# Optimization experiments

Measured on AMD Instinct MI355X. Metric: run time of the kernel, lower is better.

Reference implementation:

```python
import jax, jax.numpy as jnp
import numpy as np

N, E, B = 2048, 65536, 8
H, G, F, S, MH, L = 128, 50, 64, 16, 32, 2
K = 512                       # = master_rate * N
CUTOFF = 10.0
TAU = 1.0
LAMBDA_ATTN = 0.002
OFFSET = jnp.linspace(0.0, CUTOFF, G)
COEFF = -0.5 / (CUTOFF / (G - 1)) ** 2


def ssp(x):
    # shifted softplus used by SchNet
    return jax.nn.softplus(x) - jnp.log(2.0)


def gauss(d):
    # GaussianSmearing: exp(coeff * (d - offset)^2)
    return jnp.exp(COEFF * (d[..., None] - OFFSET) ** 2)


def ccut(d):
    # cosine cutoff of CFConv
    return 0.5 * (jnp.cos(d * jnp.pi / CUTOFF) + 1.0)


def dist(a, b):
    # eps keeps sqrt grad finite at coincident points / self edges
    return jnp.sqrt(jnp.sum((a - b) ** 2, axis=-1) + 1e-12)


def filt(ea, mw1, mb1, mw2, mb2):
    # CFConv filter network on edge_attr
    return ssp(ea @ mw1 + mb1) @ mw2 + mb2


def hmp_layer(h, pos, src, dst, p):
    (mw1, mb1, mw2, mb2, cf1, cf2w, cf2b, lw, lb,
     aw1, ab1, aw2, ab2, msw1, msb1, msw2, msb2, wq, wk) = p
    # ---- local SchNet interaction over the full edge list (decay = 1) ----
    d = dist(pos[src], pos[dst])                                    # [E]
    W = filt(gauss(d), mw1, mb1, mw2, mb2) * ccut(d)[:, None]       # [E,F]
    x = h @ cf1                                                     # [N,F]
    agg = jnp.zeros((N, F), h.dtype).at[dst].add(x[src] * W)
    h_local = h + (ssp(agg @ cf2w + cf2b) @ lw + lb)
    # ---- master selection (top-K on scalar channels, soft sigmoid gate) ----
    hs = h_local[:, :S]
    scores = jax.nn.relu(hs @ msw1 + msb1) @ msw2 + msb2            # [N]
    topv, topi = jax.lax.top_k(scores, K)
    m = jax.nn.sigmoid((scores - topv[K - 1] + 1e-6) / TAU)         # m>0.5 exactly for masters
    midx = jnp.sort(topi)
    is_m = jnp.zeros((N,), bool).at[midx].set(True)
    inv = jnp.zeros((N,), jnp.int32).at[midx].set(jnp.arange(K, dtype=jnp.int32))
    valid = is_m[src] & is_m[dst]                                   # induced-subgraph edges
    srcm = jnp.where(valid, inv[src], 0)
    dstm = jnp.where(valid, inv[dst], 0)
    vf = valid.astype(h.dtype)
    adj = jnp.zeros((K, K), h.dtype).at[srcm, dstm].add(vf) > 0     # to_dense_adj
    h_m, pos_m = h_local[midx], pos[midx]
    # ---- virtual edge generation (dot-product attention, thresholded) ----
    hms = h_m[:, :S]
    attn = jax.nn.softmax((hms @ wq) @ (hms @ wk).T / jnp.sqrt(jnp.asarray(S, h.dtype)), axis=-1)
    Av = ((attn > LAMBDA_ATTN) & ~adj & ~jnp.eye(K, dtype=bool)).astype(h.dtype)  # [K,K]
    # ---- master interaction: induced edges (sparse) + virtual edges (dense) ----
    dm = dist(pos_m[srcm], pos_m[dstm])
    Wm = filt(gauss(dm), mw1, mb1, mw2, mb2) * (ccut(dm) * vf)[:, None]
    xm = h_m @ cf1                                                  # [K,F]
    agg_s = jnp.zeros((K, F), h.dtype).at[dstm].add(xm[srcm] * Wm)
    dmat = dist(pos_m[:, None, :], pos_m[None, :, :])               # [K,K]
    gmat = gauss(dmat)                                              # [K,K,G]
    Wi, Wj, Wd = aw1[:H], aw1[H:2 * H], aw1[2 * H:]                 # split concat-MLP first layer
    pre = jax.nn.relu((h_m @ Wi)[:, None, :] + (h_m @ Wj)[None, :, :] + gmat @ Wd + ab1)
    score = pre @ aw2 + ab2                                         # [K,K] attn_mlp score
    # scatter_softmax grouped by source row over existing virtual edges
    decay = jax.nn.softmax(jnp.where(Av > 0, score, -1e9), axis=1) * Av
    Wv = filt(gmat * decay[..., None], mw1, mb1, mw2, mb2) * (ccut(dmat) * Av)[..., None]
    agg_d = jnp.einsum('if,ijf->jf', xm, Wv)                        # aggregate at target col
    h_hier = h_m + (ssp((agg_s + agg_d) @ cf2w + cf2b) @ lw + lb)
    h_exp = jnp.zeros_like(h_local).at[midx].set(h_hier)
    mc = m[:, None]
    return (1.0 - mc) * h_local + mc * h_exp


def reference(atoms, pos, src, dst, batch, emb,
              ib_mlp_w1, ib_mlp_b1, ib_mlp_w2, ib_mlp_b2,
              cf_lin1_w, cf_lin2_w, cf_lin2_b, ib_lin_w, ib_lin_b,
              attn_w1, attn_b1, attn_w2, attn_b2,
              ms_w1, ms_b1, ms_w2, ms_b2, vg_wq, vg_wk,
              pred_w1, pred_b1, pred_w2, pred_b2):
    ps = (ib_mlp_w1, ib_mlp_b1, ib_mlp_w2, ib_mlp_b2,
          cf_lin1_w, cf_lin2_w, cf_lin2_b, ib_lin_w, ib_lin_b,
          attn_w1, attn_b1, attn_w2, attn_b2,
          ms_w1, ms_b1, ms_w2, ms_b2, vg_wq, vg_wk)
    h = emb[atoms]
    for l in range(L):
        h = hmp_layer(h, pos, src, dst, tuple(q[l] for q in ps))
    pooled = jax.ops.segment_sum(h, batch, num_segments=B)          # global_add_pool
    return jax.nn.silu(pooled @ pred_w1 + pred_b1) @ pred_w2 + pred_b2


def setup_inputs():
    key = jax.random.key(0)
    ks = jax.random.split(key, 20)
    def rn(i, shape, s):
        return jax.random.normal(ks[i], shape, jnp.float32) * s
    return {
        'atoms': jax.random.randint(ks[0], (N,), 0, 100),
        'pos': jax.random.normal(ks[1], (N, 3), jnp.float32) * 3.0,
        'src': jax.random.randint(ks[2], (E,), 0, N),
        'dst': jax.random.randint(ks[3], (E,), 0, N),
        'batch': (jnp.arange(N) * B) // N,
        'emb': rn(4, (100, H), 0.5),
        'ib_mlp_w1': rn(5, (L, G, F), 0.1),
        'ib_mlp_b1': jnp.zeros((L, F), jnp.float32),
        'ib_mlp_w2': rn(6, (L, F, F), 0.1),
        'ib_mlp_b2': jnp.zeros((L, F), jnp.float32),
        'cf_lin1_w': rn(7, (L, H, F), 0.05),
        'cf_lin2_w': rn(8, (L, F, H), 0.05),
        'cf_lin2_b': jnp.zeros((L, H), jnp.float32),
        'ib_lin_w': rn(9, (L, H, H), 0.05),
        'ib_lin_b': jnp.zeros((L, H), jnp.float32),
        'attn_w1': rn(10, (L, 2 * H + G, H), 0.05),
        'attn_b1': jnp.zeros((L, H), jnp.float32),
        'attn_w2': rn(11, (L, H), 0.05),
        'attn_b2': jnp.zeros((L,), jnp.float32),
        'ms_w1': rn(12, (L, S, MH), 0.2),
        'ms_b1': jnp.zeros((L, MH), jnp.float32),
        'ms_w2': rn(13, (L, MH), 0.2),
        'ms_b2': jnp.zeros((L,), jnp.float32),
        'vg_wq': rn(14, (L, S, S), 0.2),
        'vg_wk': rn(15, (L, S, S), 0.2),
        'pred_w1': rn(16, (H, H // 2), 0.05),
        'pred_b1': jnp.zeros((H // 2,), jnp.float32),
        'pred_w2': rn(17, (H // 2, 1), 0.05),
        'pred_b2': jnp.zeros((1,), jnp.float32),
    }
```

## Files before the change

### kernel.cpp

```cpp
#include <hip/hip_runtime.h>
#include <hip/hip_bf16.h>
#include <math.h>

#define N_ATOMS 2048
#define E_EDGES 65536
#define B_BATCH 8
#define H_DIM 128
#define G_DIM 50
#define F_DIM 64
#define S_DIM 16
#define MH_DIM 32
#define K_TOP 512
#define L_LAYERS 2
#define EPW2 8
#define PCHUNK 8
#define NB 4096
#define DD 0.015625f
#define INV_DD 64.0f

static constexpr float STEP   = 10.0f / 49.0f;
static constexpr float COEFF  = -12.005f;
static constexpr float PI10   = 0.31415926535897931f;
static constexpr float LN2    = 0.69314718055994531f;
static constexpr float LAMBDA = 0.002f;

#define DEV static __device__ __forceinline__

DEV float ssp_f(float x) { return fmaxf(x, 0.f) + log1pf(expf(-fabsf(x))) - LN2; }
DEV float ccut_f(float d) { return 0.5f * (cosf(d * PI10) + 1.f); }
DEV float sigm_f(float x) { return 1.f / (1.f + expf(-x)); }
DEV float ssp_fast(float x) { return fmaxf(x, 0.f) + __logf(1.f + __expf(-fabsf(x))) - LN2; }
DEV float ccut_fast(float d) { return 0.5f * (__cosf(d * PI10) + 1.f); }

__global__ __launch_bounds__(256) void k_detect(const unsigned short* raw, int n, int* flag) {
    __shared__ int any;
    if (threadIdx.x == 0) any = 0;
    __syncthreads();
    for (int i = threadIdx.x; i < n; i += 256) {
        unsigned int bits = ((unsigned int)raw[i]) << 16;
        float f = __uint_as_float(bits);
        if (!(fabsf(f) <= 1e10f)) any = 1;
    }
    __syncthreads();
    if (threadIdx.x == 0) flag[0] = any;
}

struct ConvArgs {
    const void* p[25];
    int off[26];
};

__global__ __launch_bounds__(256) void k_convert_all(ConvArgs a, float* dst, const int* flag) {
    int i = blockIdx.x * 256 + threadIdx.x;
    int total = a.off[25];
    if (i >= total) return;
    int seg = 0;
    while (i >= a.off[seg + 1]) seg++;
    int k = i - a.off[seg];
    if (flag[0]) {
        dst[i] = ((const float*)a.p[seg])[k];
    } else {
        unsigned int bits = ((unsigned int)((const unsigned short*)a.p[seg])[k]) << 16;
        dst[i] = __uint_as_float(bits);
    }
}

__global__ __launch_bounds__(256) void k_ehist(const int* dst, int* hist) {
    int e = blockIdx.x * 256 + threadIdx.x;
    atomicAdd(&hist[dst[e]], 1);
}

__global__ __launch_bounds__(1024) void k_escan(const int* hist, int* ebase, int* ecur) {
    __shared__ int bufA[N_ATOMS], bufB[N_ATOMS];
    int t = threadIdx.x;
    for (int i = t; i < N_ATOMS; i += 1024) bufA[i] = hist[i];
    __syncthreads();
    int* in = bufA;
    int* out = bufB;
    for (int d = 1; d < N_ATOMS; d <<= 1) {
        for (int i = t; i < N_ATOMS; i += 1024) out[i] = in[i] + (i >= d ? in[i - d] : 0);
        __syncthreads();
        int* tmp = in; in = out; out = tmp;
    }
    for (int i = t; i < N_ATOMS; i += 1024) {
        int ex = in[i] - hist[i];
        ebase[i] = ex;
        ecur[i] = ex;
    }
}

__global__ __launch_bounds__(256) void k_escatter(const int* dst, int* ecur, int* esorted) {
    int e = blockIdx.x * 256 + threadIdx.x;
    int pos = atomicAdd(&ecur[dst[e]], 1);
    esorted[pos] = e;
}

__global__ __launch_bounds__(256) void k_edat(const int* esorted, const int* src, const int* dst,
                                              const float* pos, int4* edat) {
    int p = blockIdx.x * 256 + threadIdx.x;
    int e = esorted[p];
    int s = src[e], d = dst[e];
    float dx = pos[s * 3 + 0] - pos[d * 3 + 0];
    float dy = pos[s * 3 + 1] - pos[d * 3 + 1];
    float dz = pos[s * 3 + 2] - pos[d * 3 + 2];
    float dist = sqrtf(dx * dx + dy * dy + dz * dz + 1e-12f);
    edat[p] = make_int4(s, d, __float_as_int(dist), 0);
}

__global__ __launch_bounds__(128) void k_ftab(const float* mw1, const float* mb1,
                                              const float* mw2, const float* mb2,
                                              const float* aw1,
                                              float* z1tab, float* wtab, float* ztabS) {
    __shared__ float gs[G_DIM];
    __shared__ float tb[F_DIM];
    int b = blockIdx.x, t = threadIdx.x;
    float d = b * DD;
    if (t < G_DIM) { float u = d - t * STEP; gs[t] = expf(COEFF * u * u); }
    __syncthreads();
    const float* wd = aw1 + 2 * H_DIM * H_DIM;
    float zs = 0.f;
    for (int g = 0; g < G_DIM; g++) zs += gs[g] * wd[g * H_DIM + t];
    ztabS[b * H_DIM + t] = zs;
    if (t < F_DIM) {
        float z1 = 0.f;
        for (int g = 0; g < G_DIM; g++) z1 += gs[g] * mw1[g * F_DIM + t];
        z1tab[b * F_DIM + t] = z1;
        tb[t] = ssp_f(z1 + mb1[t]);
    }
    __syncthreads();
    if (t < F_DIM) {
        float w = mb2[t];
        for (int k = 0; k < F_DIM; k++) w += tb[k] * mw2[k * F_DIM + t];
        wtab[b * F_DIM + t] = w * ccut_f(d);
    }
}

__global__ __launch_bounds__(256) void k_embed(const int* atoms, const float* emb, float* h) {
    int i = blockIdx.x * 256 + threadIdx.x;
    int n = i >> 7, c = i & 127;
    h[i] = emb[atoms[n] * H_DIM + c];
}

__global__ __launch_bounds__(256) void k_x(const float* __restrict__ h, const float* __restrict__ cf1,
                                           float* __restrict__ x, float* __restrict__ aggz, int M) {
    int wave = threadIdx.x >> 6, lane = threadIdx.x & 63;
    int n = blockIdx.x * 4 + wave;
    if (n >= M) return;
    float acc = 0.f;
    for (int k = 0; k < H_DIM; k++) acc += h[n * H_DIM + k] * cf1[k * F_DIM + lane];
    x[n * F_DIM + lane] = acc;
    aggz[n * F_DIM + lane] = 0.f;
}

__global__ __launch_bounds__(256) void k_edge_s(const int4* edat, const float* x,
                                                const float* __restrict__ wtab,
                                                float* agg) {
    int t = threadIdx.x, wave = t >> 6, lane = t & 63;
    int p0 = (blockIdx.x * 4 + wave) * EPW2;
    int curDst = -1;
    float acc = 0.f;
    for (int ee = 0; ee < EPW2; ee++) {
        int4 ed = edat[p0 + ee];
        int sI = ed.x, dI = ed.y;
        float d = __int_as_float(ed.z);
        float s = d * INV_DD;
        int b0 = min((int)s, NB - 2);
        float fr = s - b0;
        float w0 = wtab[b0 * F_DIM + lane];
        float w1 = wtab[(b0 + 1) * F_DIM + lane];
        float w = w0 + fr * (w1 - w0);
        float contrib = x[sI * F_DIM + lane] * w;
        if (dI != curDst) {
            if (curDst >= 0) atomicAdd(&agg[curDst * F_DIM + lane], acc);
            acc = 0.f;
            curDst = dI;
        }
        acc += contrib;
    }
    if (curDst >= 0) atomicAdd(&agg[curDst * F_DIM + lane], acc);
}

__global__ __launch_bounds__(256) void k_update(const float* __restrict__ agg, const float* __restrict__ base,
                                                const float* cf2w, const float* cf2b,
                                                const float* lw, const float* lb,
                                                float* out, int M) {
    __shared__ float tbuf[4][H_DIM];
    int wave = threadIdx.x >> 6, lane = threadIdx.x & 63;
    int n = blockIdx.x * 4 + wave;
    float t0 = cf2b[lane], t1 = cf2b[lane + 64];
    if (n < M) {
        for (int f = 0; f < F_DIM; f++) {
            float a = agg[n * F_DIM + f];
            t0 += a * cf2w[f * H_DIM + lane];
            t1 += a * cf2w[f * H_DIM + lane + 64];
        }
    }
    tbuf[wave][lane] = ssp_f(t0);
    tbuf[wave][lane + 64] = ssp_f(t1);
    __syncthreads();
    if (n < M) {
        float o0 = lb[lane], o1 = lb[lane + 64];
        const float4* t4v = (const float4*)tbuf[wave];
        #pragma unroll
        for (int kk = 0; kk < 32; kk++) {
            float4 tq = t4v[kk];
            int k4 = kk * 4;
            o0 += tq.x * lw[(k4 + 0) * H_DIM + lane];
            o1 += tq.x * lw[(k4 + 0) * H_DIM + lane + 64];
            o0 += tq.y * lw[(k4 + 1) * H_DIM + lane];
            o1 += tq.y * lw[(k4 + 1) * H_DIM + lane + 64];
            o0 += tq.z * lw[(k4 + 2) * H_DIM + lane];
            o1 += tq.z * lw[(k4 + 2) * H_DIM + lane + 64];
            o0 += tq.w * lw[(k4 + 3) * H_DIM + lane];
            o1 += tq.w * lw[(k4 + 3) * H_DIM + lane + 64];
        }
        out[n * H_DIM + lane]      = base[n * H_DIM + lane] + o0;
        out[n * H_DIM + lane + 64] = base[n * H_DIM + lane + 64] + o1;
    }
}

__global__ __launch_bounds__(256) void k_scores(const float* h_local,
                                                const float* msw1, const float* msb1,
                                                const float* msw2, const float* msb2,
                                                float* scores) {
    int n = blockIdx.x * 256 + threadIdx.x;
    if (n >= N_ATOMS) return;
    float hs[S_DIM];
    for (int s = 0; s < S_DIM; s++) hs[s] = h_local[n * H_DIM + s];
    float sc = msb2[0];
    for (int j = 0; j < MH_DIM; j++) {
        float v = msb1[j];
        for (int s = 0; s < S_DIM; s++) v += hs[s] * msw1[s * MH_DIM + j];
        sc += fmaxf(v, 0.f) * msw2[j];
    }
    scores[n] = sc;
}

__global__ __launch_bounds__(256) void k_rank(const float* scores, int* rank) {
    __shared__ float s[N_ATOMS];
    __shared__ int pc[16][17];
    int t = threadIdx.x;
    for (int i = t; i < N_ATOMS; i += 256) s[i] = scores[i];
    __syncthreads();
    int ii = t & 15, chunk = t >> 4;
    int i = blockIdx.x * 16 + ii;
    float si = s[i];
    int cnt = 0;
    int j0 = chunk * (N_ATOMS / 16);
    #pragma unroll 4
    for (int j = j0; j < j0 + N_ATOMS / 16; j++) {
        float sj = s[j];
        cnt += (sj > si) || (sj == si && j < i);
    }
    pc[chunk][ii] = cnt;
    __syncthreads();
    if (chunk == 0) {
        int r = 0;
        #pragma unroll
        for (int c = 0; c < 16; c++) r += pc[c][ii];
        rank[i] = r;
    }
}

__global__ __launch_bounds__(1024) void k_select(const float* scores, const int* rank,
                                                 int* is_m, int* invg, int* midx, float* m) {
    __shared__ int flag[N_ATOMS];
    __shared__ int bufA[N_ATOMS], bufB[N_ATOMS];
    __shared__ float kth;
    int t = threadIdx.x;
    for (int i = t; i < N_ATOMS; i += 1024) {
        int f = rank[i] < K_TOP;
        flag[i] = f;
        bufA[i] = f;
        if (rank[i] == K_TOP - 1) kth = scores[i];
    }
    __syncthreads();
    int* in = bufA;
    int* out = bufB;
    for (int d = 1; d < N_ATOMS; d <<= 1) {
        for (int i = t; i < N_ATOMS; i += 1024) out[i] = in[i] + (i >= d ? in[i - d] : 0);
        __syncthreads();
        int* tmp = in; in = out; out = tmp;
    }
    float kv = kth;
    for (int i = t; i < N_ATOMS; i += 1024) {
        int f = flag[i];
        int pos = in[i] - f;
        is_m[i] = f;
        invg[i] = f ? pos : 0;
        if (f) midx[pos] = i;
        m[i] = sigm_f(scores[i] - kv + 1e-6f);
    }
}

__global__ __launch_bounds__(256) void k_gather(const int* midx, const float* h_local,
                                                const float* pos, float* h_m, float* pos_m,
                                                unsigned char* adj) {
    int i = blockIdx.x * 256 + threadIdx.x;
    int k = i >> 7, c = i & 127;
    int n = midx[k];
    h_m[i] = h_local[n * H_DIM + c];
    if (c < 3) pos_m[k * 3 + c] = pos[n * 3 + c];
    adj[i] = 0;
}

__global__ __launch_bounds__(256) void k_adj(const int* src, const int* dst, const int* is_m,
                                             const int* invg, unsigned char* adj,
                                             int* velist, int* nve) {
    int e = blockIdx.x * 256 + threadIdx.x;
    int s = src[e], d = dst[e];
    bool valid = is_m[s] && is_m[d];
    if (valid) adj[invg[s] * K_TOP + invg[d]] = 1;
    unsigned long long mask = __ballot(valid);
    int lane = threadIdx.x & 63;
    int cnt = __popcll(mask);
    int base = 0;
    if (lane == 0 && cnt) base = atomicAdd(nve, cnt);
    base = __shfl(base, 0);
    if (valid) velist[base + __popcll(mask & ((1ull << lane) - 1))] = e;
}

__global__ __launch_bounds__(256) void k_vdat(const int* velist, const int* nve,
                                              const int* src, const int* dst, const int* invg,
                                              const float* pos_m, int4* vdat) {
    int n = nve[0];
    for (int p = blockIdx.x * 256 + threadIdx.x; p < n; p += gridDim.x * 256) {
        int e = velist[p];
        int sm = invg[src[e]];
        int dm = invg[dst[e]];
        float dx = pos_m[sm * 3 + 0] - pos_m[dm * 3 + 0];
        float dy = pos_m[sm * 3 + 1] - pos_m[dm * 3 + 1];
        float dz = pos_m[sm * 3 + 2] - pos_m[dm * 3 + 2];
        float dist = sqrtf(dx * dx + dy * dy + dz * dz + 1e-12f);
        vdat[p] = make_int4(sm, dm, __float_as_int(dist), 0);
    }
}

__global__ __launch_bounds__(256) void k_qk(const float* h_m, const float* wq,
                                            const float* wk, float* qm, float* km) {
    int gid = blockIdx.x * 256 + threadIdx.x;
    int r = gid >> 5, t = gid & 31;
    const float* w = (t < 16) ? wq : wk;
    int c = t & 15;
    float acc = 0.f;
    for (int s = 0; s < S_DIM; s++) acc += h_m[r * H_DIM + s] * w[s * S_DIM + c];
    if (t < 16) qm[r * S_DIM + c] = acc; else km[r * S_DIM + c] = acc;
}

__global__ __launch_bounds__(256) void k_attn(const float* qm, const float* km,
                                              const unsigned char* adj, unsigned char* Av) {
    __shared__ float lrow[K_TOP];
    __shared__ float red[256];
    int i = blockIdx.x, t = threadIdx.x;
    float q[S_DIM];
    for (int s = 0; s < S_DIM; s++) q[s] = qm[i * S_DIM + s];
    for (int j = t; j < K_TOP; j += 256) {
        float acc = 0.f;
        for (int s = 0; s < S_DIM; s++) acc += q[s] * km[j * S_DIM + s];
        lrow[j] = acc * 0.25f;
    }
    __syncthreads();
    float mx = -1e30f;
    for (int j = t; j < K_TOP; j += 256) mx = fmaxf(mx, lrow[j]);
    red[t] = mx; __syncthreads();
    for (int o = 128; o > 0; o >>= 1) { if (t < o) red[t] = fmaxf(red[t], red[t + o]); __syncthreads(); }
    mx = red[0]; __syncthreads();
    float sum = 0.f;
    for (int j = t; j < K_TOP; j += 256) sum += expf(lrow[j] - mx);
    red[t] = sum; __syncthreads();
    for (int o = 128; o > 0; o >>= 1) { if (t < o) red[t] += red[t + o]; __syncthreads(); }
    float inv_s = 1.f / red[0];
    for (int j = t; j < K_TOP; j += 256) {
        float a = expf(lrow[j] - mx) * inv_s;
        Av[i * K_TOP + j] = (a > LAMBDA) && (!adj[i * K_TOP + j]) && (i != j);
    }
}

__global__ __launch_bounds__(256) void k_pcount(const unsigned char* Av, int* bcount) {
    __shared__ int wsum[4];
    int idx = blockIdx.x * 256 + threadIdx.x;
    int j = idx >> 9, i = idx & (K_TOP - 1);
    bool act = Av[i * K_TOP + j] != 0;
    unsigned long long mask = __ballot(act);
    int lane = threadIdx.x & 63, wave = threadIdx.x >> 6;
    if (lane == 0) wsum[wave] = __popcll(mask);
    __syncthreads();
    if (threadIdx.x == 0) bcount[blockIdx.x] = wsum[0] + wsum[1] + wsum[2] + wsum[3];
}

__global__ __launch_bounds__(1024) void k_pscan(const int* bcount, int* boffset, int* total) {
    __shared__ int bufA[1024], bufB[1024];
    int t = threadIdx.x;
    bufA[t] = bcount[t];
    __syncthreads();
    int* in = bufA;
    int* out = bufB;
    for (int d = 1; d < 1024; d <<= 1) {
        out[t] = in[t] + (t >= d ? in[t - d] : 0);
        __syncthreads();
        int* tmp = in; in = out; out = tmp;
    }
    boffset[t] = in[t] - bcount[t];
    if (t == 1023) total[0] = in[1023];
}

__global__ __launch_bounds__(256) void k_pscatter(const unsigned char* Av, const int* boffset,
                                                  unsigned int* plist) {
    __shared__ int wsum[4], woff[4];
    int idx = blockIdx.x * 256 + threadIdx.x;
    int j = idx >> 9, i = idx & (K_TOP - 1);
    bool act = Av[i * K_TOP + j] != 0;
    unsigned long long mask = __ballot(act);
    int lane = threadIdx.x & 63, wave = threadIdx.x >> 6;
    if (lane == 0) wsum[wave] = __popcll(mask);
    __syncthreads();
    if (threadIdx.x == 0) {
        int s = 0;
        for (int w = 0; w < 4; w++) { woff[w] = s; s += wsum[w]; }
    }
    __syncthreads();
    if (act) {
        int pos = boffset[blockIdx.x] + woff[wave] + __popcll(mask & ((1ull << lane) - 1));
        plist[pos] = ((unsigned int)j << 9) | (unsigned int)i;
    }
}

__global__ __launch_bounds__(256) void k_sdata(const unsigned int* plist, const int* npairs,
                                               const float* pos_m, float2* sd) {
    int n = npairs[0];
    for (int p = blockIdx.x * 256 + threadIdx.x; p < n; p += gridDim.x * 256) {
        unsigned int key = plist[p];
        int j = key >> 9, i = key & (K_TOP - 1);
        float dx = pos_m[i * 3 + 0] - pos_m[j * 3 + 0];
        float dy = pos_m[i * 3 + 1] - pos_m[j * 3 + 1];
        float dz = pos_m[i * 3 + 2] - pos_m[j * 3 + 2];
        float dd = sqrtf(dx * dx + dy * dy + dz * dz + 1e-12f);
        sd[p] = make_float2(__uint_as_float(key), dd);
    }
}

__global__ __launch_bounds__(256) void k_pdat(const unsigned int* plist, const int* npairs,
                                              const float* pos_m, const float* decay, float4* pd,
                                              float* agg_m) {
    int gid = blockIdx.x * 256 + threadIdx.x;
    if (gid < K_TOP * F_DIM) agg_m[gid] = 0.f;
    int n = npairs[0];
    for (int p = gid; p < n; p += gridDim.x * 256) {
        unsigned int key = plist[p];
        int j = key >> 9, i = key & (K_TOP - 1);
        float dx = pos_m[i * 3 + 0] - pos_m[j * 3 + 0];
        float dy = pos_m[i * 3 + 1] - pos_m[j * 3 + 1];
        float dz = pos_m[i * 3 + 2] - pos_m[j * 3 + 2];
        float dd = sqrtf(dx * dx + dy * dy + dz * dz + 1e-12f);
        pd[p] = make_float4(__uint_as_float(key), dd, decay[i * K_TOP + j], 0.f);
    }
}

__global__ __launch_bounds__(256) void k_hij(const float* h_m, const float* aw1,
                                             float* hi, float* hj) {
    int wave = threadIdx.x >> 6, lane = threadIdx.x & 63;
    int idx = blockIdx.x * 4 + wave;
    int which = idx >> 9;
    int r = idx & (K_TOP - 1);
    const float* W = aw1 + which * H_DIM * H_DIM;
    float o0 = 0.f, o1 = 0.f;
    for (int k = 0; k < H_DIM; k++) {
        float hv = h_m[r * H_DIM + k];
        o0 += hv * W[k * H_DIM + lane];
        o1 += hv * W[k * H_DIM + lane + 64];
    }
    float* out = which ? hj : hi;
    out[r * H_DIM + lane] = o0;
    out[r * H_DIM + lane + 64] = o1;
}

__global__ __launch_bounds__(256) void k_score_p(const float2* sd, const int* npairs,
                                                 const float* hi, const float* hj,
                                                 const float* __restrict__ ztabS,
                                                 const float* ab1, const float* aw2, const float* ab2,
                                                 float* sbuf) {
    int t = threadIdx.x, wave = t >> 6, lane = t & 63;
    float ab0 = ab1[lane], ab1v = ab1[lane + 64];
    float aw0 = aw2[lane], aw1v = aw2[lane + 64];
    float b2 = ab2[0];
    int n = npairs[0];
    int wid = blockIdx.x * 4 + wave;
    int nw = gridDim.x * 4;
    for (int p = wid; p < n; p += nw) {
        float2 s2 = sd[p];
        unsigned int key = __float_as_uint(s2.x);
        float dd = s2.y;
        int j = key >> 9, i = key & (K_TOP - 1);
        int ij = i * K_TOP + j;
        float s = dd * INV_DD;
        int b0 = min((int)s, NB - 2);
        float fr = s - b0;
        const float* r0 = ztabS + b0 * H_DIM;
        const float* r1 = r0 + H_DIM;
        float z0a = r0[lane],      z1a = r1[lane];
        float z0b = r0[lane + 64], z1b = r1[lane + 64];
        float zs0 = z0a + fr * (z1a - z0a);
        float zs1 = z0b + fr * (z1b - z0b);
        float v0 = hi[i * H_DIM + lane] + hj[j * H_DIM + lane] + ab0 + zs0;
        float v1 = hi[i * H_DIM + lane + 64] + hj[j * H_DIM + lane + 64] + ab1v + zs1;
        float pv = fmaxf(v0, 0.f) * aw0 + fmaxf(v1, 0.f) * aw1v;
        for (int o = 1; o < 64; o <<= 1) pv += __shfl_xor(pv, o);
        if (lane == 0) sbuf[ij] = pv + b2;
    }
}

__global__ __launch_bounds__(256) void k_decay(const float* sbuf, const unsigned char* Av, float* decay) {
    __shared__ float srow[K_TOP];
    __shared__ float red[256];
    int i = blockIdx.x, t = threadIdx.x;
    for (int j = t; j < K_TOP; j += 256)
        srow[j] = Av[i * K_TOP + j] ? sbuf[i * K_TOP + j] : -1e9f;
    __syncthreads();
    float mx = -1e30f;
    for (int j = t; j < K_TOP; j += 256) mx = fmaxf(mx, srow[j]);
    red[t] = mx; __syncthreads();
    for (int o = 128; o > 0; o >>= 1) { if (t < o) red[t] = fmaxf(red[t], red[t + o]); __syncthreads(); }
    mx = red[0]; __syncthreads();
    float sum = 0.f;
    for (int j = t; j < K_TOP; j += 256) sum += (srow[j] > -5e8f) ? expf(srow[j] - mx) : 0.f;
    red[t] = sum; __syncthreads();
    for (int o = 128; o > 0; o >>= 1) { if (t < o) red[t] += red[t + o]; __syncthreads(); }
    float s_total = red[0];
    float inv_s = (s_total > 0.f) ? 1.f / s_total : 0.f;
    for (int j = t; j < K_TOP; j += 256)
        decay[i * K_TOP + j] = (srow[j] > -5e8f) ? expf(srow[j] - mx) * inv_s : 0.f;
}

__global__ __launch_bounds__(256) void k_aggd_p2(const float4* pd, const int* npairs,
                                                 const float* xm,
                                                 const float* __restrict__ z1tab,
                                                 const float* mb1,
                                                 const float* mw2, const float* mb2,
                                                 float* agg_m) {
    __shared__ float tbuf[4][F_DIM];
    int t = threadIdx.x, wave = t >> 6, lane = t & 63;
    float w2r[F_DIM];
    #pragma unroll
    for (int k = 0; k < F_DIM; k++) w2r[k] = mw2[k * F_DIM + lane];
    float b1 = mb1[lane], b2v = mb2[lane];
    int n = npairs[0];
    int nchunks = (n + PCHUNK - 1) / PCHUNK;
    int wid = blockIdx.x * 4 + wave;
    int nw = gridDim.x * 4;
    for (int c = wid; c < nchunks; c += nw) {
        int p0 = c * PCHUNK;
        int p1 = min(p0 + PCHUNK, n);
        int curJ = -1;
        float acc = 0.f;
        for (int p = p0; p < p1; p++) {
            float4 q = pd[p];
            unsigned int key = __float_as_uint(q.x);
            float dd = q.y, dec = q.z;
            int j = key >> 9, i = key & (K_TOP - 1);
            float s = dd * INV_DD;
            int b0 = min((int)s, NB - 2);
            float fr = s - b0;
            float z0 = z1tab[b0 * F_DIM + lane];
            float z1 = z1tab[(b0 + 1) * F_DIM + lane];
            float z1v = z0 + fr * (z1 - z0);
            float tv = ssp_fast(dec * z1v + b1);
            tbuf[wave][lane] = tv;
            float w = b2v;
            const float4* t4v = (const float4*)tbuf[wave];
            #pragma unroll
            for (int kk = 0; kk < 16; kk++) {
                float4 tq = t4v[kk];
                w += tq.x * w2r[4 * kk + 0];
                w += tq.y * w2r[4 * kk + 1];
                w += tq.z * w2r[4 * kk + 2];
                w += tq.w * w2r[4 * kk + 3];
            }
            float contrib = xm[i * F_DIM + lane] * w * ccut_fast(dd);
            if (j != curJ) {
                if (curJ >= 0) atomicAdd(&agg_m[curJ * F_DIM + lane], acc);
                acc = 0.f;
                curJ = j;
            }
            acc += contrib;
        }
        if (curJ >= 0) atomicAdd(&agg_m[curJ * F_DIM + lane], acc);
    }
}

__global__ __launch_bounds__(256) void k_aggs_p(const int4* vdat, const int* nve,
                                                const float* xm,
                                                const float* __restrict__ wtab,
                                                float* agg_m) {
    int t = threadIdx.x, wave = t >> 6, lane = t & 63;
    int n = nve[0];
    int wid = blockIdx.x * 4 + wave;
    int nw = gridDim.x * 4;
    for (int p = wid; p < n; p += nw) {
        int4 vd = vdat[p];
        int sm = vd.x, dm = vd.y;
        float d = __int_as_float(vd.z);
        float s = d * INV_DD;
        int b0 = min((int)s, NB - 2);
        float fr = s - b0;
        float w0 = wtab[b0 * F_DIM + lane];
        float w1 = wtab[(b0 + 1) * F_DIM + lane];
        float w = w0 + fr * (w1 - w0);
        atomicAdd(&agg_m[dm * F_DIM + lane], xm[sm * F_DIM + lane] * w);
    }
}

__global__ __launch_bounds__(256) void k_blend(const float* h_local, const float* h_hier,
                                               const int* is_m, const int* invg, const float* m,
                                               float* h_out) {
    int idx = blockIdx.x * 256 + threadIdx.x;
    int n = idx >> 7, c = idx & 127;
    float mm = m[n];
    float hh = is_m[n] ? h_hier[invg[n] * H_DIM + c] : 0.f;
    h_out[idx] = (1.f - mm) * h_local[idx] + mm * hh;
}

__global__ __launch_bounds__(256) void k_pool(const float* __restrict__ h, const int* __restrict__ batch,
                                              float* pooled) {
    int c = threadIdx.x & 127, a = threadIdx.x >> 7;
    int n0 = blockIdx.x * 64;
    float acc = 0.f;
    int cur = batch[n0 + a];
    for (int i = a; i < 64; i += 2) {
        int n = n0 + i;
        int b = batch[n];
        if (b != cur) { atomicAdd(&pooled[cur * H_DIM + c], acc); acc = 0.f; cur = b; }
        acc += h[n * H_DIM + c];
    }
    atomicAdd(&pooled[cur * H_DIM + c], acc);
}

__global__ __launch_bounds__(128) void k_pred2(const float* pooled,
                                               const float* w1, const float* b1,
                                               const float* w2, const float* b2,
                                               void* outv, const int* flag) {
    __shared__ float c64[64];
    int b = blockIdx.x, t = threadIdx.x;
    if (t < 64) {
        float v = b1[t];
        for (int k = 0; k < H_DIM; k++) v += pooled[b * H_DIM + k] * w1[k * 64 + t];
        c64[t] = v * sigm_f(v);
    }
    __syncthreads();
    if (t == 0) {
        float o = b2[0];
        for (int k = 0; k < 64; k++) o += c64[k] * w2[k];
        if (flag[0]) ((float*)outv)[b] = o;
        else ((__hip_bfloat16*)outv)[b] = __float2bfloat16(o);
    }
}

extern "C" void kernel_launch(void* const* d_in, const int* in_sizes, int n_in,
                              void* d_out, int out_size, void* d_ws, size_t ws_size,
                              hipStream_t stream) {
    (void)n_in; (void)out_size; (void)ws_size;
    const int* atoms = (const int*)d_in[0];
    const int* src = (const int*)d_in[2];
    const int* dst = (const int*)d_in[3];
    const int* batch = (const int*)d_in[4];

    float* W = (float*)d_ws;
    int* dflag = (int*)W; W += 16;
    int* counters = (int*)W; W += 16;

    static const int fidx[25] = {1,5,6,7,8,9,10,11,12,13,14,15,16,17,18,19,20,21,22,23,24,25,26,27,28};
    float* fin[29];
    ConvArgs ca;
    float* convBase = W;
    int off = 0;
    for (int q = 0; q < 25; q++) {
        int i = fidx[q];
        ca.p[q] = d_in[i];
        ca.off[q] = off;
        fin[i] = convBase + off;
        off += in_sizes[i];
    }
    ca.off[25] = off;
    W += off;

    k_detect<<<1, 256, 0, stream>>>((const unsigned short*)d_in[5], in_sizes[5], dflag);
    k_convert_all<<<(off + 255) / 256, 256, 0, stream>>>(ca, convBase, dflag);

    const float* posf = fin[1];
    const float* embf = fin[5];

    float* h      = W; W += N_ATOMS * H_DIM;
    float* h_loc  = W; W += N_ATOMS * H_DIM;
    float* xbuf   = W; W += N_ATOMS * F_DIM;
    float* aggbuf = W; W += N_ATOMS * F_DIM;
    float* scores = W; W += N_ATOMS;
    float* mbuf   = W; W += N_ATOMS;
    float* h_m    = W; W += K_TOP * H_DIM;
    float* pos_m  = W; W += K_TOP * 3;
    float* xm     = W; W += K_TOP * F_DIM;
    float* qm     = W; W += K_TOP * S_DIM;
    float* km     = W; W += K_TOP * S_DIM;
    float* decay  = W; W += K_TOP * K_TOP;
    float* sbuf   = W; W += K_TOP * K_TOP;
    float* hi     = W; W += K_TOP * H_DIM;
    float* hj     = W; W += K_TOP * H_DIM;
    float* agg_m  = W; W += K_TOP * F_DIM;
    float* h_hier = W; W += K_TOP * H_DIM;
    float* pooled = W; W += B_BATCH * H_DIM;
    float* z1tab  = W; W += NB * F_DIM;
    float* wtab   = W; W += NB * F_DIM;
    float* ztabS  = W; W += NB * H_DIM;
    int* rankb  = (int*)W; W += N_ATOMS;
    int* is_m   = (int*)W; W += N_ATOMS;
    int* invg   = (int*)W; W += N_ATOMS;
    int* midx   = (int*)W; W += K_TOP;
    unsigned int* plist = (unsigned int*)W; W += K_TOP * K_TOP;
    int* velist = (int*)W; W += E_EDGES;
    int* esorted = (int*)W; W += E_EDGES;
    int* ehist  = (int*)W; W += N_ATOMS;
    int* ebase  = (int*)W; W += N_ATOMS;
    int* ecur   = (int*)W; W += N_ATOMS;
    int* bcount = (int*)W; W += 1024;
    int* boffset = (int*)W; W += 1024;
    int4* edat  = (int4*)W; W += E_EDGES * 4;
    int4* vdat  = (int4*)W; W += E_EDGES * 4;
    float2* sd  = (float2*)W; W += K_TOP * K_TOP * 2;
    float4* pd  = (float4*)W; W += K_TOP * K_TOP * 4;
    unsigned char* adj = (unsigned char*)W; W += (K_TOP * K_TOP) / 4;
    unsigned char* Av  = (unsigned char*)W; W += (K_TOP * K_TOP) / 4;

    (void)hipMemsetAsync(ehist, 0, N_ATOMS * sizeof(int), stream);
    k_ehist<<<E_EDGES / 256, 256, 0, stream>>>(dst, ehist);
    k_escan<<<1, 1024, 0, stream>>>(ehist, ebase, ecur);
    k_escatter<<<E_EDGES / 256, 256, 0, stream>>>(dst, ecur, esorted);
    k_edat<<<E_EDGES / 256, 256, 0, stream>>>(esorted, src, dst, posf, edat);

    k_embed<<<(N_ATOMS * H_DIM) / 256, 256, 0, stream>>>(atoms, embf, h);

    for (int l = 0; l < L_LAYERS; l++) {
        const float* mw1 = fin[6]  + l * G_DIM * F_DIM;
        const float* mb1 = fin[7]  + l * F_DIM;
        const float* mw2 = fin[8]  + l * F_DIM * F_DIM;
        const float* mb2 = fin[9]  + l * F_DIM;
        const float* cf1 = fin[10] + l * H_DIM * F_DIM;
        const float* cf2w = fin[11] + l * F_DIM * H_DIM;
        const float* cf2b = fin[12] + l * H_DIM;
        const float* lw  = fin[13] + l * H_DIM * H_DIM;
        const float* lb  = fin[14] + l * H_DIM;
        const float* aw1 = fin[15] + l * (2 * H_DIM + G_DIM) * H_DIM;
        const float* ab1 = fin[16] + l * H_DIM;
        const float* aw2 = fin[17] + l * H_DIM;
        const float* ab2 = fin[18] + l;
        const float* msw1 = fin[19] + l * S_DIM * MH_DIM;
        const float* msb1 = fin[20] + l * MH_DIM;
        const float* msw2 = fin[21] + l * MH_DIM;
        const float* msb2 = fin[22] + l;
        const float* wq  = fin[23] + l * S_DIM * S_DIM;
        const float* wk  = fin[24] + l * S_DIM * S_DIM;

        k_ftab<<<NB, 128, 0, stream>>>(mw1, mb1, mw2, mb2, aw1, z1tab, wtab, ztabS);
        k_x<<<N_ATOMS / 4, 256, 0, stream>>>(h, cf1, xbuf, aggbuf, N_ATOMS);
        k_edge_s<<<E_EDGES / (4 * EPW2), 256, 0, stream>>>(edat, xbuf, wtab, aggbuf);
        k_update<<<N_ATOMS / 4, 256, 0, stream>>>(aggbuf, h, cf2w, cf2b, lw, lb, h_loc, N_ATOMS);
        k_scores<<<N_ATOMS / 256, 256, 0, stream>>>(h_loc, msw1, msb1, msw2, msb2, scores);
        k_rank<<<N_ATOMS / 16, 256, 0, stream>>>(scores, rankb);
        k_select<<<1, 1024, 0, stream>>>(scores, rankb, is_m, invg, midx, mbuf);
        k_gather<<<(K_TOP * H_DIM) / 256, 256, 0, stream>>>(midx, h_loc, posf, h_m, pos_m, adj);
        k_x<<<K_TOP / 4, 256, 0, stream>>>(h_m, cf1, xm, agg_m, K_TOP);
        (void)hipMemsetAsync(counters, 0, 2 * sizeof(int), stream);
        k_adj<<<E_EDGES / 256, 256, 0, stream>>>(src, dst, is_m, invg, adj, velist, counters + 1);
        k_vdat<<<256, 256, 0, stream>>>(velist, counters + 1, src, dst, invg, pos_m, vdat);
        k_qk<<<(K_TOP * 32) / 256, 256, 0, stream>>>(h_m, wq, wk, qm, km);
        k_attn<<<K_TOP, 256, 0, stream>>>(qm, km, adj, Av);
        k_pcount<<<(K_TOP * K_TOP) / 256, 256, 0, stream>>>(Av, bcount);
        k_pscan<<<1, 1024, 0, stream>>>(bcount, boffset, counters);
        k_pscatter<<<(K_TOP * K_TOP) / 256, 256, 0, stream>>>(Av, boffset, plist);
        k_sdata<<<512, 256, 0, stream>>>(plist, counters, pos_m, sd);
        k_hij<<<(2 * K_TOP) / 4, 256, 0, stream>>>(h_m, aw1, hi, hj);
        k_score_p<<<1024, 256, 0, stream>>>(sd, counters, hi, hj, ztabS, ab1, aw2, ab2, sbuf);
        k_decay<<<K_TOP, 256, 0, stream>>>(sbuf, Av, decay);
        k_pdat<<<512, 256, 0, stream>>>(plist, counters, pos_m, decay, pd, agg_m);
        k_aggd_p2<<<4096, 256, 0, stream>>>(pd, counters, xm, z1tab, mb1, mw2, mb2, agg_m);
        k_aggs_p<<<256, 256, 0, stream>>>(vdat, counters + 1, xm, wtab, agg_m);
        k_update<<<K_TOP / 4, 256, 0, stream>>>(agg_m, h_m, cf2w, cf2b, lw, lb, h_hier, K_TOP);
        k_blend<<<(N_ATOMS * H_DIM) / 256, 256, 0, stream>>>(h_loc, h_hier, is_m, invg, mbuf, h);
    }

    (void)hipMemsetAsync(pooled, 0, B_BATCH * H_DIM * sizeof(float), stream);
    k_pool<<<N_ATOMS / 64, 256, 0, stream>>>(h, batch, pooled);
    k_pred2<<<B_BATCH, 128, 0, stream>>>(pooled, fin[25], fin[26], fin[27], fin[28], d_out, dflag);
}
```

Before: 368.9 us.

## Fuse small master-selection and pair-list kernels to cut launches and serial scan

Replaces the single-block prefix-scan selection with a 128-block counting kernel, with the kth score now recorded by the rank kernel. Moves the counter memset into the gather kernel and folds virtual-edge data construction into the adjacency kernel. Merges the hi/hj projection with the q/k projection and folds pair-distance computation into the pair scatter. The pdat kernel now reuses the stored distances instead of recomputing them. This removes several launches and one serial single-block stage per layer. In exchange the selection does O(N^2) redundant rank comparisons, and agg_m zeroing now relies on k_x.

```diff
diff --git a/kernel.cpp b/kernel.cpp
--- a/kernel.cpp
+++ b/kernel.cpp
@@ -236,7 +236,7 @@
     scores[n] = sc;
 }
 
-__global__ __launch_bounds__(256) void k_rank(const float* scores, int* rank) {
+__global__ __launch_bounds__(256) void k_rank(const float* scores, int* rank, float* kvbuf) {
     __shared__ float s[N_ATOMS];
     __shared__ int pc[16][17];
     int t = threadIdx.x;
@@ -259,92 +259,103 @@
         #pragma unroll
         for (int c = 0; c < 16; c++) r += pc[c][ii];
         rank[i] = r;
-    }
-}
-
-__global__ __launch_bounds__(1024) void k_select(const float* scores, const int* rank,
+        if (r == K_TOP - 1) kvbuf[0] = si;
+    }
+}
+
+__global__ __launch_bounds__(256) void k_select2(const float* scores, const int* rank,
+                                                 const float* kvbuf,
                                                  int* is_m, int* invg, int* midx, float* m) {
-    __shared__ int flag[N_ATOMS];
-    __shared__ int bufA[N_ATOMS], bufB[N_ATOMS];
-    __shared__ float kth;
+    __shared__ int rk[N_ATOMS];
+    __shared__ int pc[16][17];
     int t = threadIdx.x;
-    for (int i = t; i < N_ATOMS; i += 1024) {
-        int f = rank[i] < K_TOP;
-        flag[i] = f;
-        bufA[i] = f;
-        if (rank[i] == K_TOP - 1) kth = scores[i];
-    }
-    __syncthreads();
-    int* in = bufA;
-    int* out = bufB;
-    for (int d = 1; d < N_ATOMS; d <<= 1) {
-        for (int i = t; i < N_ATOMS; i += 1024) out[i] = in[i] + (i >= d ? in[i - d] : 0);
-        __syncthreads();
-        int* tmp = in; in = out; out = tmp;
-    }
-    float kv = kth;
-    for (int i = t; i < N_ATOMS; i += 1024) {
-        int f = flag[i];
-        int pos = in[i] - f;
+    for (int i = t; i < N_ATOMS; i += 256) rk[i] = rank[i];
+    __syncthreads();
+    int ii = t & 15, chunk = t >> 4;
+    int i = blockIdx.x * 16 + ii;
+    int j0 = chunk * (N_ATOMS / 16);
+    int cnt = 0;
+    #pragma unroll 4
+    for (int j = j0; j < j0 + N_ATOMS / 16; j++)
+        cnt += (j < i && rk[j] < K_TOP);
+    pc[chunk][ii] = cnt;
+    __syncthreads();
+    if (chunk == 0) {
+        int pos = 0;
+        #pragma unroll
+        for (int c = 0; c < 16; c++) pos += pc[c][ii];
+        int f = rk[i] < K_TOP;
         is_m[i] = f;
         invg[i] = f ? pos : 0;
         if (f) midx[pos] = i;
-        m[i] = sigm_f(scores[i] - kv + 1e-6f);
+        m[i] = sigm_f(scores[i] - kvbuf[0] + 1e-6f);
     }
 }
 
 __global__ __launch_bounds__(256) void k_gather(const int* midx, const float* h_local,
                                                 const float* pos, float* h_m, float* pos_m,
-                                                unsigned char* adj) {
+                                                unsigned char* adj, int* counters) {
     int i = blockIdx.x * 256 + threadIdx.x;
     int k = i >> 7, c = i & 127;
     int n = midx[k];
     h_m[i] = h_local[n * H_DIM + c];
     if (c < 3) pos_m[k * 3 + c] = pos[n * 3 + c];
     adj[i] = 0;
+    if (i < 2) counters[i] = 0;
 }
 
 __global__ __launch_bounds__(256) void k_adj(const int* src, const int* dst, const int* is_m,
-                                             const int* invg, unsigned char* adj,
-                                             int* velist, int* nve) {
+                                             const int* invg, const float* pos_m,
+                                             unsigned char* adj, int4* vdat, int* nve) {
     int e = blockIdx.x * 256 + threadIdx.x;
     int s = src[e], d = dst[e];
     bool valid = is_m[s] && is_m[d];
-    if (valid) adj[invg[s] * K_TOP + invg[d]] = 1;
+    int sm = valid ? invg[s] : 0;
+    int dm = valid ? invg[d] : 0;
+    if (valid) adj[sm * K_TOP + dm] = 1;
     unsigned long long mask = __ballot(valid);
     int lane = threadIdx.x & 63;
     int cnt = __popcll(mask);
     int base = 0;
     if (lane == 0 && cnt) base = atomicAdd(nve, cnt);
     base = __shfl(base, 0);
-    if (valid) velist[base + __popcll(mask & ((1ull << lane) - 1))] = e;
-}
-
-__global__ __launch_bounds__(256) void k_vdat(const int* velist, const int* nve,
-                                              const int* src, const int* dst, const int* invg,
-                                              const float* pos_m, int4* vdat) {
-    int n = nve[0];
-    for (int p = blockIdx.x * 256 + threadIdx.x; p < n; p += gridDim.x * 256) {
-        int e = velist[p];
-        int sm = invg[src[e]];
-        int dm = invg[dst[e]];
+    if (valid) {
+        int pos = base + __popcll(mask & ((1ull << lane) - 1));
         float dx = pos_m[sm * 3 + 0] - pos_m[dm * 3 + 0];
         float dy = pos_m[sm * 3 + 1] - pos_m[dm * 3 + 1];
         float dz = pos_m[sm * 3 + 2] - pos_m[dm * 3 + 2];
         float dist = sqrtf(dx * dx + dy * dy + dz * dz + 1e-12f);
-        vdat[p] = make_int4(sm, dm, __float_as_int(dist), 0);
-    }
-}
-
-__global__ __launch_bounds__(256) void k_qk(const float* h_m, const float* wq,
-                                            const float* wk, float* qm, float* km) {
-    int gid = blockIdx.x * 256 + threadIdx.x;
-    int r = gid >> 5, t = gid & 31;
-    const float* w = (t < 16) ? wq : wk;
-    int c = t & 15;
-    float acc = 0.f;
-    for (int s = 0; s < S_DIM; s++) acc += h_m[r * H_DIM + s] * w[s * S_DIM + c];
-    if (t < 16) qm[r * S_DIM + c] = acc; else km[r * S_DIM + c] = acc;
+        vdat[pos] = make_int4(sm, dm, __float_as_int(dist), 0);
+    }
+}
+
+__global__ __launch_bounds__(256) void k_hijqk(const float* h_m, const float* aw1,
+                                               const float* wq, const float* wk,
+                                               float* hi, float* hj, float* qm, float* km) {
+    if (blockIdx.x < 256) {
+        int wave = threadIdx.x >> 6, lane = threadIdx.x & 63;
+        int idx = blockIdx.x * 4 + wave;
+        int which = idx >> 9;
+        int r = idx & (K_TOP - 1);
+        const float* W = aw1 + which * H_DIM * H_DIM;
+        float o0 = 0.f, o1 = 0.f;
+        for (int k = 0; k < H_DIM; k++) {
+            float hv = h_m[r * H_DIM + k];
+            o0 += hv * W[k * H_DIM + lane];
+            o1 += hv * W[k * H_DIM + lane + 64];
+        }
+        float* out = which ? hj : hi;
+        out[r * H_DIM + lane] = o0;
+        out[r * H_DIM + lane + 64] = o1;
+    } else {
+        int gid = (blockIdx.x - 256) * 256 + threadIdx.x;
+        int r = gid >> 5, t = gid & 31;
+        const float* w = (t < 16) ? wq : wk;
+        int c = t & 15;
+        float acc = 0.f;
+        for (int s = 0; s < S_DIM; s++) acc += h_m[r * H_DIM + s] * w[s * S_DIM + c];
+        if (t < 16) qm[r * S_DIM + c] = acc; else km[r * S_DIM + c] = acc;
+    }
 }
 
 __global__ __launch_bounds__(256) void k_attn(const float* qm, const float* km,
@@ -405,7 +416,8 @@
 }
 
 __global__ __launch_bounds__(256) void k_pscatter(const unsigned char* Av, const int* boffset,
-                                                  unsigned int* plist) {
+                                                  const float* pos_m,
+                                                  unsigned int* plist, float2* sd) {
     __shared__ int wsum[4], woff[4];
     int idx = blockIdx.x * 256 + threadIdx.x;
     int j = idx >> 9, i = idx & (K_TOP - 1);
@@ -421,57 +433,14 @@
     __syncthreads();
     if (act) {
         int pos = boffset[blockIdx.x] + woff[wave] + __popcll(mask & ((1ull << lane) - 1));
-        plist[pos] = ((unsigned int)j << 9) | (unsigned int)i;
-    }
-}
-
-__global__ __launch_bounds__(256) void k_sdata(const unsigned int* plist, const int* npairs,
-                                               const float* pos_m, float2* sd) {
-    int n = npairs[0];
-    for (int p = blockIdx.x * 256 + threadIdx.x; p < n; p += gridDim.x * 256) {
-        unsigned int key = plist[p];
-        int j = key >> 9, i = key & (K_TOP - 1);
+        unsigned int key = ((unsigned int)j << 9) | (unsigned int)i;
+        plist[pos] = key;
         float dx = pos_m[i * 3 + 0] - pos_m[j * 3 + 0];
         float dy = pos_m[i * 3 + 1] - pos_m[j * 3 + 1];
         float dz = pos_m[i * 3 + 2] - pos_m[j * 3 + 2];
         float dd = sqrtf(dx * dx + dy * dy + dz * dz + 1e-12f);
-        sd[p] = make_float2(__uint_as_float(key), dd);
-    }
-}
-
-__global__ __launch_bounds__(256) void k_pdat(const unsigned int* plist, const int* npairs,
-                                              const float* pos_m, const float* decay, float4* pd,
-                                              float* agg_m) {
-    int gid = blockIdx.x * 256 + threadIdx.x;
-    if (gid < K_TOP * F_DIM) agg_m[gid] = 0.f;
-    int n = npairs[0];
-    for (int p = gid; p < n; p += gridDim.x * 256) {
-        unsigned int key = plist[p];
-        int j = key >> 9, i = key & (K_TOP - 1);
-        float dx = pos_m[i * 3 + 0] - pos_m[j * 3 + 0];
-        float dy = pos_m[i * 3 + 1] - pos_m[j * 3 + 1];
-        float dz = pos_m[i * 3 + 2] - pos_m[j * 3 + 2];
-        float dd = sqrtf(dx * dx + dy * dy + dz * dz + 1e-12f);
-        pd[p] = make_float4(__uint_as_float(key), dd, decay[i * K_TOP + j], 0.f);
-    }
-}
-
-__global__ __launch_bounds__(256) void k_hij(const float* h_m, const float* aw1,
-                                             float* hi, float* hj) {
-    int wave = threadIdx.x >> 6, lane = threadIdx.x & 63;
-    int idx = blockIdx.x * 4 + wave;
-    int which = idx >> 9;
-    int r = idx & (K_TOP - 1);
-    const float* W = aw1 + which * H_DIM * H_DIM;
-    float o0 = 0.f, o1 = 0.f;
-    for (int k = 0; k < H_DIM; k++) {
-        float hv = h_m[r * H_DIM + k];
-        o0 += hv * W[k * H_DIM + lane];
-        o1 += hv * W[k * H_DIM + lane + 64];
-    }
-    float* out = which ? hj : hi;
-    out[r * H_DIM + lane] = o0;
-    out[r * H_DIM + lane + 64] = o1;
+        sd[pos] = make_float2(__uint_as_float(key), dd);
+    }
 }
 
 __global__ __launch_bounds__(256) void k_score_p(const float2* sd, const int* npairs,
@@ -529,6 +498,17 @@
     float inv_s = (s_total > 0.f) ? 1.f / s_total : 0.f;
     for (int j = t; j < K_TOP; j += 256)
         decay[i * K_TOP + j] = (srow[j] > -5e8f) ? expf(srow[j] - mx) * inv_s : 0.f;
+}
+
+__global__ __launch_bounds__(256) void k_pdat(const float2* sd, const int* npairs,
+                                              const float* decay, float4* pd) {
+    int n = npairs[0];
+    for (int p = blockIdx.x * 256 + threadIdx.x; p < n; p += gridDim.x * 256) {
+        float2 s2 = sd[p];
+        unsigned int key = __float_as_uint(s2.x);
+        int j = key >> 9, i = key & (K_TOP - 1);
+        pd[p] = make_float4(s2.x, s2.y, decay[i * K_TOP + j], 0.f);
+    }
 }
 
 __global__ __launch_bounds__(256) void k_aggd_p2(const float4* pd, const int* npairs,
@@ -666,6 +646,7 @@
     float* W = (float*)d_ws;
     int* dflag = (int*)W; W += 16;
     int* counters = (int*)W; W += 16;
+    float* kvbuf = (float*)(counters + 4);
 
     static const int fidx[25] = {1,5,6,7,8,9,10,11,12,13,14,15,16,17,18,19,20,21,22,23,24,25,26,27,28};
     float* fin[29];
@@ -714,7 +695,6 @@
     int* invg   = (int*)W; W += N_ATOMS;
     int* midx   = (int*)W; W += K_TOP;
     unsigned int* plist = (unsigned int*)W; W += K_TOP * K_TOP;
-    int* velist = (int*)W; W += E_EDGES;
     int* esorted = (int*)W; W += E_EDGES;
     int* ehist  = (int*)W; W += N_ATOMS;
     int* ebase  = (int*)W; W += N_ATOMS;
@@ -762,23 +742,19 @@
         k_edge_s<<<E_EDGES / (4 * EPW2), 256, 0, stream>>>(edat, xbuf, wtab, aggbuf);
         k_update<<<N_ATOMS / 4, 256, 0, stream>>>(aggbuf, h, cf2w, cf2b, lw, lb, h_loc, N_ATOMS);
         k_scores<<<N_ATOMS / 256, 256, 0, stream>>>(h_loc, msw1, msb1, msw2, msb2, scores);
-        k_rank<<<N_ATOMS / 16, 256, 0, stream>>>(scores, rankb);
-        k_select<<<1, 1024, 0, stream>>>(scores, rankb, is_m, invg, midx, mbuf);
-        k_gather<<<(K_TOP * H_DIM) / 256, 256, 0, stream>>>(midx, h_loc, posf, h_m, pos_m, adj);
+        k_rank<<<N_ATOMS / 16, 256, 0, stream>>>(scores, rankb, kvbuf);
+        k_select2<<<N_ATOMS / 16, 256, 0, stream>>>(scores, rankb, kvbuf, is_m, invg, midx, mbuf);
+        k_gather<<<(K_TOP * H_DIM) / 256, 256, 0, stream>>>(midx, h_loc, posf, h_m, pos_m, adj, counters);
         k_x<<<K_TOP / 4, 256, 0, stream>>>(h_m, cf1, xm, agg_m, K_TOP);
-        (void)hipMemsetAsync(counters, 0, 2 * sizeof(int), stream);
-        k_adj<<<E_EDGES / 256, 256, 0, stream>>>(src, dst, is_m, invg, adj, velist, counters + 1);
-        k_vdat<<<256, 256, 0, stream>>>(velist, counters + 1, src, dst, invg, pos_m, vdat);
-        k_qk<<<(K_TOP * 32) / 256, 256, 0, stream>>>(h_m, wq, wk, qm, km);
+        k_adj<<<E_EDGES / 256, 256, 0, stream>>>(src, dst, is_m, invg, pos_m, adj, vdat, counters + 1);
+        k_hijqk<<<320, 256, 0, stream>>>(h_m, aw1, wq, wk, hi, hj, qm, km);
         k_attn<<<K_TOP, 256, 0, stream>>>(qm, km, adj, Av);
         k_pcount<<<(K_TOP * K_TOP) / 256, 256, 0, stream>>>(Av, bcount);
         k_pscan<<<1, 1024, 0, stream>>>(bcount, boffset, counters);
-        k_pscatter<<<(K_TOP * K_TOP) / 256, 256, 0, stream>>>(Av, boffset, plist);
-        k_sdata<<<512, 256, 0, stream>>>(plist, counters, pos_m, sd);
-        k_hij<<<(2 * K_TOP) / 4, 256, 0, stream>>>(h_m, aw1, hi, hj);
+        k_pscatter<<<(K_TOP * K_TOP) / 256, 256, 0, stream>>>(Av, boffset, pos_m, plist, sd);
         k_score_p<<<1024, 256, 0, stream>>>(sd, counters, hi, hj, ztabS, ab1, aw2, ab2, sbuf);
         k_decay<<<K_TOP, 256, 0, stream>>>(sbuf, Av, decay);
-        k_pdat<<<512, 256, 0, stream>>>(plist, counters, pos_m, decay, pd, agg_m);
+        k_pdat<<<512, 256, 0, stream>>>(sd, counters, decay, pd);
         k_aggd_p2<<<4096, 256, 0, stream>>>(pd, counters, xm, z1tab, mb1, mw2, mb2, agg_m);
         k_aggs_p<<<256, 256, 0, stream>>>(vdat, counters + 1, xm, wtab, agg_m);
         k_update<<<K_TOP / 4, 256, 0, stream>>>(agg_m, h_m, cf2w, cf2b, lw, lb, h_hier, K_TOP);
```

New measurement: 360.5 us. 2.3% less time.
